# Optimization experiments

Hardware: AMD Instinct MI355X
Metric: run time of the kernel (lower is better)

The kernel has to match this reference:

```python
import jax, jax.numpy as jnp
import numpy as np

NEG_INF = -1.0e9
VALID_THRESH = -1.0e8
EPS = 1e-12


def _l2_normalize(x):
    n = jnp.linalg.norm(x, axis=-1, keepdims=True)
    return x / jnp.maximum(n, EPS)


def setup_inputs() -> dict:
    key = jax.random.key(0)
    k1, k2, k3, k4 = jax.random.split(key, 4)
    B, Nq, Nd, D = 64, 32, 256, 128
    return {
        "query_embeds": jax.random.normal(k1, (B, Nq, D), dtype=jnp.float32),
        "query_mask": jax.random.randint(k2, (B, Nq), 0, 2, dtype=jnp.int32),
        "doc_embeds": jax.random.normal(k3, (B, Nd, D), dtype=jnp.float32),
        "doc_mask": jax.random.randint(k4, (B, Nd), 0, 2, dtype=jnp.int32),
    }


def reference(query_embeds, query_mask, doc_embeds, doc_mask):
    # normalize=True, symmetric=True path
    q = _l2_normalize(query_embeds)
    d = _l2_normalize(doc_embeds)
    qm = query_mask.astype(jnp.float32)[..., None]  # [B, Nq, 1]
    dm = doc_mask.astype(jnp.float32)[..., None]    # [B, Nd, 1]
    q = q * qm
    d = d * dm

    # token_sims: [Bq, Bd, Nq, Nd]
    token_sims = jnp.einsum("qtd,csd->qcts", q, d)
    # pair mask: [Bq,1,Nq,1] * [1,Bd,1,Nd]
    mask = qm[:, None, :, :] * dm[None, :, :, 0][:, :, None, :].transpose(1, 0, 2, 3)
    masked_sims = jnp.where(mask > 0, token_sims, NEG_INF)

    # query -> doc max over doc tokens
    q2d = jnp.max(masked_sims, axis=-1)          # [Bq, Bd, Nq]
    valid_q = (q2d > VALID_THRESH).astype(jnp.float32)
    q2d = jnp.where(valid_q > 0, q2d, 0.0)
    cnt_q = jnp.maximum(jnp.sum(valid_q, axis=-1), 1.0)
    q2d_score = jnp.sum(q2d, axis=-1) / cnt_q    # [Bq, Bd]

    # doc -> query max over query tokens
    d2q = jnp.max(masked_sims, axis=-2)          # [Bq, Bd, Nd]
    valid_d = (d2q > VALID_THRESH).astype(jnp.float32)
    d2q = jnp.where(valid_d > 0, d2q, 0.0)
    cnt_d = jnp.maximum(jnp.sum(valid_d, axis=-1), 1.0)
    d2q_score = jnp.sum(d2q, axis=-1) / cnt_d    # [Bq, Bd]

    return (q2d_score + d2q_score) / 2.0
```

## Files before the change

### kernel.cpp

```cpp
#include <hip/hip_runtime.h>
#include <hip/hip_bf16.h>
#include <stdint.h>

typedef short bf16x8 __attribute__((ext_vector_type(8)));
typedef short short8 __attribute__((ext_vector_type(8)));
typedef float f32x4 __attribute__((ext_vector_type(4)));

#define B_   64
#define NQ   32
#define ND   256
#define DIM  128
#define MT   4
#define NEG_INF_F (-1.0e9f)
#define VALID_F   (-1.0e8f)


__device__ __forceinline__ void lds_cp16(const void* g, void* l) {
    __builtin_amdgcn_global_load_lds(
        (const __attribute__((address_space(1))) unsigned int*)g,
        (__attribute__((address_space(3))) unsigned int*)l,
        16, 0, 0);
}

__global__ __launch_bounds__(256) void normalize_rows(
    const float* __restrict__ q, const int* __restrict__ qmask,
    const float* __restrict__ d, const int* __restrict__ dmask,
    __hip_bfloat16* __restrict__ qn, __hip_bfloat16* __restrict__ dn)
{
    const int tid  = threadIdx.x;
    const int sub  = tid & 15;
    const int row  = blockIdx.x * 16 + (tid >> 4);

    const float* src;
    __hip_bfloat16* dst;
    int m, swz;
    if (row < B_ * NQ) {
        src = q + (size_t)row * DIM;  dst = qn + (size_t)row * DIM;
        m = qmask[row];  swz = 0;
    } else {
        const int r2 = row - B_ * NQ;
        src = d + (size_t)r2 * DIM;   dst = dn + (size_t)r2 * DIM;
        m = dmask[r2];   swz = r2 & 7;
    }

    const float4 v0 = *reinterpret_cast<const float4*>(src + sub * 8);
    const float4 v1 = *reinterpret_cast<const float4*>(src + sub * 8 + 4);
    float ss = v0.x*v0.x + v0.y*v0.y + v0.z*v0.z + v0.w*v0.w
             + v1.x*v1.x + v1.y*v1.y + v1.z*v1.z + v1.w*v1.w;
    #pragma unroll
    for (int off = 1; off <= 8; off <<= 1) ss += __shfl_xor(ss, off);

    const float scale = m ? (1.0f / fmaxf(sqrtf(ss), 1e-12f)) : 0.0f;

    short8 o;
    const float f[8] = {v0.x, v0.y, v0.z, v0.w, v1.x, v1.y, v1.z, v1.w};
    #pragma unroll
    for (int j = 0; j < 8; ++j) {
        __hip_bfloat16 b = __float2bfloat16(f[j] * scale);
        o[j] = *reinterpret_cast<short*>(&b);
    }
    *reinterpret_cast<short8*>(dst + (sub ^ swz) * 8) = o;
}

__global__ __launch_bounds__(256) void chamfer_main(
    const __hip_bfloat16* __restrict__ qn,
    const __hip_bfloat16* __restrict__ dn,
    const int* __restrict__ qmask,
    const int* __restrict__ dmask,
    float* __restrict__ out)
{
    __shared__ __hip_bfloat16 ldsD[ND * DIM];
    __shared__ float s_cmax[MT][ND];
    __shared__ float s_rmaxT[MT][NQ][4];

    const int bq0 = (blockIdx.x >> 6) * MT;
    const int bd  = blockIdx.x & 63;
    const int tid = threadIdx.x;
    const int w   = tid >> 6;
    const int l   = tid & 63;
    const int lr  = l & 15;
    const int lk  = l >> 4;

    {
        const char* gD = (const char*)(dn + (size_t)(bd * ND) * DIM) + w * 16384;
        char*       lD = (char*)&ldsD[0] + w * 16384;
        #pragma unroll
        for (int c = 0; c < 16; ++c)
            lds_cp16(gD + c * 1024 + l * 16, lD + c * 1024);
    }

    int qmv[MT][2][4];
    int dmv[MT][4];
    #pragma unroll
    for (int m = 0; m < MT; ++m) {
        #pragma unroll
        for (int mi = 0; mi < 2; ++mi)
            #pragma unroll
            for (int r = 0; r < 4; ++r)
                qmv[m][mi][r] = qmask[(bq0 + m) * NQ + mi * 16 + lk * 4 + r];
        #pragma unroll
        for (int ni = 0; ni < 4; ++ni)
            dmv[m][ni] = dmask[(bq0 + m) * ND + w * 64 + ni * 16 + lr];
    }

    __syncthreads();

    f32x4 acc[MT][2][4] = {};
    __builtin_amdgcn_s_setprio(1);
    #pragma unroll
    for (int kk = 0; kk < 4; ++kk) {
        const int k0   = kk * 32 + lk * 8;
        const int slot = (kk * 4 + lk) ^ (lr & 7);
        bf16x8 bfr[4];
        #pragma unroll
        for (int ni = 0; ni < 4; ++ni) {
            const int rowd = w * 64 + ni * 16 + lr;
            bfr[ni] = *reinterpret_cast<const bf16x8*>((const char*)&ldsD[0] + rowd * 256 + slot * 16);
        }
        #pragma unroll
        for (int m = 0; m < MT; ++m) {
            const __hip_bfloat16* Q = qn + (size_t)(bq0 + m) * (NQ * DIM);
            #pragma unroll
            for (int mi = 0; mi < 2; ++mi) {
                const bf16x8 a = *reinterpret_cast<const bf16x8*>(Q + (mi * 16 + lr) * DIM + k0);
                #pragma unroll
                for (int ni = 0; ni < 4; ++ni)
                    acc[m][mi][ni] = __builtin_amdgcn_mfma_f32_16x16x32_bf16(a, bfr[ni], acc[m][mi][ni], 0, 0, 0);
            }
        }
    }
    __builtin_amdgcn_s_setprio(0);

    #pragma unroll
    for (int m = 0; m < MT; ++m) {
        float rmax[2][4];
        float cmax[4];
        #pragma unroll
        for (int ni = 0; ni < 4; ++ni) cmax[ni] = NEG_INF_F;
        #pragma unroll
        for (int mi = 0; mi < 2; ++mi) {
            #pragma unroll
            for (int r = 0; r < 4; ++r) {
                float rm = NEG_INF_F;
                #pragma unroll
                for (int ni = 0; ni < 4; ++ni) {
                    const float v = (qmv[m][mi][r] && dmv[m][ni]) ? acc[m][mi][ni][r] : NEG_INF_F;
                    rm = fmaxf(rm, v);
                    cmax[ni] = fmaxf(cmax[ni], v);
                }
                rmax[mi][r] = rm;
            }
        }
        #pragma unroll
        for (int ni = 0; ni < 4; ++ni) {
            cmax[ni] = fmaxf(cmax[ni], __shfl_xor(cmax[ni], 16));
            cmax[ni] = fmaxf(cmax[ni], __shfl_xor(cmax[ni], 32));
        }
        if (lk == 0) {
            #pragma unroll
            for (int ni = 0; ni < 4; ++ni)
                s_cmax[m][w * 64 + ni * 16 + lr] = cmax[ni];
        }
        #pragma unroll
        for (int mi = 0; mi < 2; ++mi)
            #pragma unroll
            for (int r = 0; r < 4; ++r) {
                #pragma unroll
                for (int off = 1; off <= 8; off <<= 1)
                    rmax[mi][r] = fmaxf(rmax[mi][r], __shfl_xor(rmax[mi][r], off));
            }
        if (lr == 0) {
            #pragma unroll
            for (int mi = 0; mi < 2; ++mi)
                #pragma unroll
                for (int r = 0; r < 4; ++r)
                    s_rmaxT[m][mi * 16 + lk * 4 + r][w] = rmax[mi][r];
        }
    }
    __syncthreads();

    {
        const int m = w;
        const float4 cm = *reinterpret_cast<const float4*>(&s_cmax[m][l * 4]);
        float sd = 0.0f, cd = 0.0f;
        if (cm.x > VALID_F) { sd += cm.x; cd += 1.0f; }
        if (cm.y > VALID_F) { sd += cm.y; cd += 1.0f; }
        if (cm.z > VALID_F) { sd += cm.z; cd += 1.0f; }
        if (cm.w > VALID_F) { sd += cm.w; cd += 1.0f; }
        float sq = 0.0f, cq = 0.0f;
        if (l < NQ) {
            const float4 rm4 = *reinterpret_cast<const float4*>(&s_rmaxT[m][l][0]);
            const float v = fmaxf(fmaxf(rm4.x, rm4.y), fmaxf(rm4.z, rm4.w));
            if (v > VALID_F) { sq = v; cq = 1.0f; }
        }
        #pragma unroll
        for (int off = 1; off <= 32; off <<= 1) {
            sd += __shfl_xor(sd, off);
            cd += __shfl_xor(cd, off);
            sq += __shfl_xor(sq, off);
            cq += __shfl_xor(cq, off);
        }
        if (l == 0) {
            const float q2d = sq / fmaxf(cq, 1.0f);
            const float d2q = sd / fmaxf(cd, 1.0f);
            out[(bq0 + m) * B_ + bd] = 0.5f * (q2d + d2q);
        }
    }
}

extern "C" void kernel_launch(void* const* d_in, const int* in_sizes, int n_in,
                              void* d_out, int out_size, void* d_ws, size_t ws_size,
                              hipStream_t stream) {
    const float* q  = (const float*)d_in[0];
    const int*   qm = (const int*)d_in[1];
    const float* d  = (const float*)d_in[2];
    const int*   dm = (const int*)d_in[3];
    float* out = (float*)d_out;

    __hip_bfloat16* qn = (__hip_bfloat16*)d_ws;
    __hip_bfloat16* dn = qn + (B_ * NQ) * DIM;

    normalize_rows<<<(B_ * NQ + B_ * ND) / 16, 256, 0, stream>>>(q, qm, d, dm, qn, dn);
    chamfer_main<<<(B_ / MT) * B_, 256, 0, stream>>>(qn, dn, qm, dm, out);
}
```

Measured before the change: 107.7 us.

## Fuse doc normalization into chamfer kernel and loop over query batches per block

Doc embeddings are normalized to bf16 directly into LDS inside the main kernel, which drops the separate doc normalization pass and its workspace round trip. Each block now handles 16 query batches in four chunks, cutting the grid from 1024 to 256 blocks. The cost is redundant normalization of each doc across the four query groups and less parallelism per CU.

```diff
diff --git a/kernel.cpp b/kernel.cpp
--- a/kernel.cpp
+++ b/kernel.cpp
@@ -14,35 +14,15 @@
 #define NEG_INF_F (-1.0e9f)
 #define VALID_F   (-1.0e8f)
 
-
-__device__ __forceinline__ void lds_cp16(const void* g, void* l) {
-    __builtin_amdgcn_global_load_lds(
-        (const __attribute__((address_space(1))) unsigned int*)g,
-        (__attribute__((address_space(3))) unsigned int*)l,
-        16, 0, 0);
-}
-
-__global__ __launch_bounds__(256) void normalize_rows(
+__global__ __launch_bounds__(256) void qnorm(
     const float* __restrict__ q, const int* __restrict__ qmask,
-    const float* __restrict__ d, const int* __restrict__ dmask,
-    __hip_bfloat16* __restrict__ qn, __hip_bfloat16* __restrict__ dn)
+    __hip_bfloat16* __restrict__ qn)
 {
-    const int tid  = threadIdx.x;
-    const int sub  = tid & 15;
-    const int row  = blockIdx.x * 16 + (tid >> 4);
-
-    const float* src;
-    __hip_bfloat16* dst;
-    int m, swz;
-    if (row < B_ * NQ) {
-        src = q + (size_t)row * DIM;  dst = qn + (size_t)row * DIM;
-        m = qmask[row];  swz = 0;
-    } else {
-        const int r2 = row - B_ * NQ;
-        src = d + (size_t)r2 * DIM;   dst = dn + (size_t)r2 * DIM;
-        m = dmask[r2];   swz = r2 & 7;
-    }
-
+    const int tid = threadIdx.x;
+    const int sub = tid & 15;
+    const int row = blockIdx.x * 16 + (tid >> 4);
+
+    const float* src = q + (size_t)row * DIM;
     const float4 v0 = *reinterpret_cast<const float4*>(src + sub * 8);
     const float4 v1 = *reinterpret_cast<const float4*>(src + sub * 8 + 4);
     float ss = v0.x*v0.x + v0.y*v0.y + v0.z*v0.z + v0.w*v0.w
@@ -50,7 +30,7 @@
     #pragma unroll
     for (int off = 1; off <= 8; off <<= 1) ss += __shfl_xor(ss, off);
 
-    const float scale = m ? (1.0f / fmaxf(sqrtf(ss), 1e-12f)) : 0.0f;
+    const float scale = qmask[row] ? (1.0f / fmaxf(sqrtf(ss), 1e-12f)) : 0.0f;
 
     short8 o;
     const float f[8] = {v0.x, v0.y, v0.z, v0.w, v1.x, v1.y, v1.z, v1.w};
@@ -59,12 +39,12 @@
         __hip_bfloat16 b = __float2bfloat16(f[j] * scale);
         o[j] = *reinterpret_cast<short*>(&b);
     }
-    *reinterpret_cast<short8*>(dst + (sub ^ swz) * 8) = o;
+    *reinterpret_cast<short8*>(qn + (size_t)row * DIM + sub * 8) = o;
 }
 
-__global__ __launch_bounds__(256) void chamfer_main(
+__global__ __launch_bounds__(256) void chamfer_fused(
+    const float* __restrict__ d,
     const __hip_bfloat16* __restrict__ qn,
-    const __hip_bfloat16* __restrict__ dn,
     const int* __restrict__ qmask,
     const int* __restrict__ dmask,
     float* __restrict__ out)
@@ -73,8 +53,8 @@
     __shared__ float s_cmax[MT][ND];
     __shared__ float s_rmaxT[MT][NQ][4];
 
-    const int bq0 = (blockIdx.x >> 6) * MT;
     const int bd  = blockIdx.x & 63;
+    const int g   = blockIdx.x >> 6;
     const int tid = threadIdx.x;
     const int w   = tid >> 6;
     const int l   = tid & 63;
@@ -82,129 +62,149 @@
     const int lk  = l >> 4;
 
     {
-        const char* gD = (const char*)(dn + (size_t)(bd * ND) * DIM) + w * 16384;
-        char*       lD = (char*)&ldsD[0] + w * 16384;
-        #pragma unroll
-        for (int c = 0; c < 16; ++c)
-            lds_cp16(gD + c * 1024 + l * 16, lD + c * 1024);
-    }
-
-    int qmv[MT][2][4];
-    int dmv[MT][4];
-    #pragma unroll
-    for (int m = 0; m < MT; ++m) {
-        #pragma unroll
-        for (int mi = 0; mi < 2; ++mi)
-            #pragma unroll
-            for (int r = 0; r < 4; ++r)
-                qmv[m][mi][r] = qmask[(bq0 + m) * NQ + mi * 16 + lk * 4 + r];
-        #pragma unroll
-        for (int ni = 0; ni < 4; ++ni)
-            dmv[m][ni] = dmask[(bq0 + m) * ND + w * 64 + ni * 16 + lr];
-    }
-
-    __syncthreads();
-
-    f32x4 acc[MT][2][4] = {};
-    __builtin_amdgcn_s_setprio(1);
-    #pragma unroll
-    for (int kk = 0; kk < 4; ++kk) {
-        const int k0   = kk * 32 + lk * 8;
-        const int slot = (kk * 4 + lk) ^ (lr & 7);
-        bf16x8 bfr[4];
-        #pragma unroll
-        for (int ni = 0; ni < 4; ++ni) {
-            const int rowd = w * 64 + ni * 16 + lr;
-            bfr[ni] = *reinterpret_cast<const bf16x8*>((const char*)&ldsD[0] + rowd * 256 + slot * 16);
-        }
-        #pragma unroll
-        for (int m = 0; m < MT; ++m) {
-            const __hip_bfloat16* Q = qn + (size_t)(bq0 + m) * (NQ * DIM);
-            #pragma unroll
-            for (int mi = 0; mi < 2; ++mi) {
-                const bf16x8 a = *reinterpret_cast<const bf16x8*>(Q + (mi * 16 + lr) * DIM + k0);
-                #pragma unroll
-                for (int ni = 0; ni < 4; ++ni)
-                    acc[m][mi][ni] = __builtin_amdgcn_mfma_f32_16x16x32_bf16(a, bfr[ni], acc[m][mi][ni], 0, 0, 0);
-            }
-        }
-    }
-    __builtin_amdgcn_s_setprio(0);
-
-    #pragma unroll
-    for (int m = 0; m < MT; ++m) {
-        float rmax[2][4];
-        float cmax[4];
-        #pragma unroll
-        for (int ni = 0; ni < 4; ++ni) cmax[ni] = NEG_INF_F;
-        #pragma unroll
-        for (int mi = 0; mi < 2; ++mi) {
-            #pragma unroll
-            for (int r = 0; r < 4; ++r) {
-                float rm = NEG_INF_F;
-                #pragma unroll
-                for (int ni = 0; ni < 4; ++ni) {
-                    const float v = (qmv[m][mi][r] && dmv[m][ni]) ? acc[m][mi][ni][r] : NEG_INF_F;
-                    rm = fmaxf(rm, v);
-                    cmax[ni] = fmaxf(cmax[ni], v);
-                }
-                rmax[mi][r] = rm;
-            }
-        }
-        #pragma unroll
-        for (int ni = 0; ni < 4; ++ni) {
-            cmax[ni] = fmaxf(cmax[ni], __shfl_xor(cmax[ni], 16));
-            cmax[ni] = fmaxf(cmax[ni], __shfl_xor(cmax[ni], 32));
-        }
-        if (lk == 0) {
-            #pragma unroll
-            for (int ni = 0; ni < 4; ++ni)
-                s_cmax[m][w * 64 + ni * 16 + lr] = cmax[ni];
-        }
-        #pragma unroll
-        for (int mi = 0; mi < 2; ++mi)
-            #pragma unroll
-            for (int r = 0; r < 4; ++r) {
-                #pragma unroll
-                for (int off = 1; off <= 8; off <<= 1)
-                    rmax[mi][r] = fmaxf(rmax[mi][r], __shfl_xor(rmax[mi][r], off));
-            }
-        if (lr == 0) {
-            #pragma unroll
-            for (int mi = 0; mi < 2; ++mi)
-                #pragma unroll
-                for (int r = 0; r < 4; ++r)
-                    s_rmaxT[m][mi * 16 + lk * 4 + r][w] = rmax[mi][r];
+        const float* Dsrc = d + (size_t)bd * ND * DIM;
+        const int sub = tid & 15;
+        const int rb  = tid >> 4;
+        #pragma unroll
+        for (int it = 0; it < 16; ++it) {
+            const int row = it * 16 + rb;
+            const float4 v0 = *reinterpret_cast<const float4*>(Dsrc + row * DIM + sub * 8);
+            const float4 v1 = *reinterpret_cast<const float4*>(Dsrc + row * DIM + sub * 8 + 4);
+            float ss = v0.x*v0.x + v0.y*v0.y + v0.z*v0.z + v0.w*v0.w
+                     + v1.x*v1.x + v1.y*v1.y + v1.z*v1.z + v1.w*v1.w;
+            #pragma unroll
+            for (int off = 1; off <= 8; off <<= 1) ss += __shfl_xor(ss, off);
+            const float scale = dmask[bd * ND + row] ? (1.0f / fmaxf(sqrtf(ss), 1e-12f)) : 0.0f;
+            short8 o;
+            const float f[8] = {v0.x, v0.y, v0.z, v0.w, v1.x, v1.y, v1.z, v1.w};
+            #pragma unroll
+            for (int j = 0; j < 8; ++j) {
+                __hip_bfloat16 b = __float2bfloat16(f[j] * scale);
+                o[j] = *reinterpret_cast<short*>(&b);
+            }
+            *reinterpret_cast<short8*>((char*)&ldsD[0] + row * 256 + ((sub ^ (row & 7)) << 4)) = o;
         }
     }
     __syncthreads();
 
-    {
-        const int m = w;
-        const float4 cm = *reinterpret_cast<const float4*>(&s_cmax[m][l * 4]);
-        float sd = 0.0f, cd = 0.0f;
-        if (cm.x > VALID_F) { sd += cm.x; cd += 1.0f; }
-        if (cm.y > VALID_F) { sd += cm.y; cd += 1.0f; }
-        if (cm.z > VALID_F) { sd += cm.z; cd += 1.0f; }
-        if (cm.w > VALID_F) { sd += cm.w; cd += 1.0f; }
-        float sq = 0.0f, cq = 0.0f;
-        if (l < NQ) {
-            const float4 rm4 = *reinterpret_cast<const float4*>(&s_rmaxT[m][l][0]);
-            const float v = fmaxf(fmaxf(rm4.x, rm4.y), fmaxf(rm4.z, rm4.w));
-            if (v > VALID_F) { sq = v; cq = 1.0f; }
-        }
-        #pragma unroll
-        for (int off = 1; off <= 32; off <<= 1) {
-            sd += __shfl_xor(sd, off);
-            cd += __shfl_xor(cd, off);
-            sq += __shfl_xor(sq, off);
-            cq += __shfl_xor(cq, off);
-        }
-        if (l == 0) {
-            const float q2d = sq / fmaxf(cq, 1.0f);
-            const float d2q = sd / fmaxf(cd, 1.0f);
-            out[(bq0 + m) * B_ + bd] = 0.5f * (q2d + d2q);
-        }
+    #pragma unroll 1
+    for (int mm = 0; mm < 4; ++mm) {
+        const int bq0 = g * 16 + mm * MT;
+
+        int4 qm4[MT][2];
+        int  dmv[MT][4];
+        #pragma unroll
+        for (int m = 0; m < MT; ++m) {
+            #pragma unroll
+            for (int mi = 0; mi < 2; ++mi)
+                qm4[m][mi] = *reinterpret_cast<const int4*>(&qmask[(bq0 + m) * NQ + mi * 16 + lk * 4]);
+            #pragma unroll
+            for (int ni = 0; ni < 4; ++ni)
+                dmv[m][ni] = dmask[(bq0 + m) * ND + w * 64 + ni * 16 + lr];
+        }
+
+        f32x4 acc[MT][2][4] = {};
+        #pragma unroll
+        for (int kk = 0; kk < 4; ++kk) {
+            const int k0   = kk * 32 + lk * 8;
+            const int cL   = kk * 4 + lk;
+            bf16x8 bfr[4];
+            #pragma unroll
+            for (int ni = 0; ni < 4; ++ni) {
+                const int rowd = w * 64 + ni * 16 + lr;
+                bfr[ni] = *reinterpret_cast<const bf16x8*>(
+                    (const char*)&ldsD[0] + rowd * 256 + ((cL ^ (rowd & 7)) << 4));
+            }
+            #pragma unroll
+            for (int m = 0; m < MT; ++m) {
+                const __hip_bfloat16* Q = qn + (size_t)(bq0 + m) * (NQ * DIM);
+                #pragma unroll
+                for (int mi = 0; mi < 2; ++mi) {
+                    const bf16x8 a = *reinterpret_cast<const bf16x8*>(Q + (mi * 16 + lr) * DIM + k0);
+                    #pragma unroll
+                    for (int ni = 0; ni < 4; ++ni)
+                        acc[m][mi][ni] = __builtin_amdgcn_mfma_f32_16x16x32_bf16(a, bfr[ni], acc[m][mi][ni], 0, 0, 0);
+                }
+            }
+        }
+
+        #pragma unroll
+        for (int m = 0; m < MT; ++m) {
+            float rmax[2][4];
+            float cmax[4];
+            #pragma unroll
+            for (int ni = 0; ni < 4; ++ni) cmax[ni] = NEG_INF_F;
+            #pragma unroll
+            for (int mi = 0; mi < 2; ++mi) {
+                const int qmr[4] = {qm4[m][mi].x, qm4[m][mi].y, qm4[m][mi].z, qm4[m][mi].w};
+                #pragma unroll
+                for (int r = 0; r < 4; ++r) {
+                    float rm = NEG_INF_F;
+                    #pragma unroll
+                    for (int ni = 0; ni < 4; ++ni) {
+                        const float v = (qmr[r] && dmv[m][ni]) ? acc[m][mi][ni][r] : NEG_INF_F;
+                        rm = fmaxf(rm, v);
+                        cmax[ni] = fmaxf(cmax[ni], v);
+                    }
+                    rmax[mi][r] = rm;
+                }
+            }
+            #pragma unroll
+            for (int ni = 0; ni < 4; ++ni) {
+                cmax[ni] = fmaxf(cmax[ni], __shfl_xor(cmax[ni], 16));
+                cmax[ni] = fmaxf(cmax[ni], __shfl_xor(cmax[ni], 32));
+            }
+            if (lk == 0) {
+                #pragma unroll
+                for (int ni = 0; ni < 4; ++ni)
+                    s_cmax[m][w * 64 + ni * 16 + lr] = cmax[ni];
+            }
+            #pragma unroll
+            for (int mi = 0; mi < 2; ++mi)
+                #pragma unroll
+                for (int r = 0; r < 4; ++r) {
+                    #pragma unroll
+                    for (int off = 1; off <= 8; off <<= 1)
+                        rmax[mi][r] = fmaxf(rmax[mi][r], __shfl_xor(rmax[mi][r], off));
+                }
+            if (lr == 0) {
+                #pragma unroll
+                for (int mi = 0; mi < 2; ++mi)
+                    #pragma unroll
+                    for (int r = 0; r < 4; ++r)
+                        s_rmaxT[m][mi * 16 + lk * 4 + r][w] = rmax[mi][r];
+            }
+        }
+        __syncthreads();
+
+        {
+            const int m = w;
+            const float4 cm = *reinterpret_cast<const float4*>(&s_cmax[m][l * 4]);
+            float sd = 0.0f, cd = 0.0f;
+            if (cm.x > VALID_F) { sd += cm.x; cd += 1.0f; }
+            if (cm.y > VALID_F) { sd += cm.y; cd += 1.0f; }
+            if (cm.z > VALID_F) { sd += cm.z; cd += 1.0f; }
+            if (cm.w > VALID_F) { sd += cm.w; cd += 1.0f; }
+            float sq = 0.0f, cq = 0.0f;
+            if (l < NQ) {
+                const float4 rm4 = *reinterpret_cast<const float4*>(&s_rmaxT[m][l][0]);
+                const float v = fmaxf(fmaxf(rm4.x, rm4.y), fmaxf(rm4.z, rm4.w));
+                if (v > VALID_F) { sq = v; cq = 1.0f; }
+            }
+            #pragma unroll
+            for (int off = 1; off <= 32; off <<= 1) {
+                sd += __shfl_xor(sd, off);
+                cd += __shfl_xor(cd, off);
+                sq += __shfl_xor(sq, off);
+                cq += __shfl_xor(cq, off);
+            }
+            if (l == 0) {
+                const float q2d = sq / fmaxf(cq, 1.0f);
+                const float d2q = sd / fmaxf(cd, 1.0f);
+                out[(bq0 + m) * B_ + bd] = 0.5f * (q2d + d2q);
+            }
+        }
+        __syncthreads();
     }
 }
 
@@ -218,8 +218,7 @@
     float* out = (float*)d_out;
 
     __hip_bfloat16* qn = (__hip_bfloat16*)d_ws;
-    __hip_bfloat16* dn = qn + (B_ * NQ) * DIM;
-
-    normalize_rows<<<(B_ * NQ + B_ * ND) / 16, 256, 0, stream>>>(q, qm, d, dm, qn, dn);
-    chamfer_main<<<(B_ / MT) * B_, 256, 0, stream>>>(qn, dn, qm, dm, out);
+
+    qnorm<<<(B_ * NQ) / 16, 256, 0, stream>>>(q, qm, qn);
+    chamfer_fused<<<B_ * 4, 256, 0, stream>>>(d, qn, qm, dm, out);
 }
```

Measured after the change: 116.0 us. 7.8% more time.
